# Kernel optimization log

Measured on AMD Instinct MI355X. Metric: run time of the kernel, lower is better.

The kernel has to match this reference:

```python
import jax, jax.numpy as jnp
import numpy as np

B, A, T, C = 8, 16, 512, 256
H = 8
DH = C // H
HID = 4 * C


def setup_inputs() -> dict:
    key = jax.random.key(0)
    ks = jax.random.split(key, 16)
    s = 0.02
    return {
        "x": jax.random.normal(ks[0], (B, A, T, C), jnp.float32),
        "ln1_w": jnp.ones((C,), jnp.float32),
        "ln1_b": jnp.zeros((C,), jnp.float32),
        "qkv_w": jax.random.normal(ks[1], (C, 3 * C), jnp.float32) * s,
        "qkv_b": jnp.zeros((3 * C,), jnp.float32),
        "proj_w": jax.random.normal(ks[2], (C, C), jnp.float32) * s,
        "proj_b": jnp.zeros((C,), jnp.float32),
        "ln2_w": jnp.ones((C,), jnp.float32),
        "ln2_b": jnp.zeros((C,), jnp.float32),
        "fc_w": jax.random.normal(ks[3], (C, HID), jnp.float32) * s,
        "fc_b": jnp.zeros((HID,), jnp.float32),
        "fc2_w": jax.random.normal(ks[4], (HID, C), jnp.float32) * s,
        "fc2_b": jnp.zeros((C,), jnp.float32),
    }


def _layernorm(x, w, b, eps=1e-5):
    mu = jnp.mean(x, axis=-1, keepdims=True)
    var = jnp.var(x, axis=-1, keepdims=True)
    return (x - mu) * jax.lax.rsqrt(var + eps) * w + b


def reference(x, ln1_w, ln1_b, qkv_w, qkv_b, proj_w, proj_b,
              ln2_w, ln2_b, fc_w, fc_b, fc2_w, fc2_b):
    # pre-LN block; note: residuals branch off the *normalized* tensor,
    # exactly as in the source forward().
    xn = _layernorm(x, ln1_w, ln1_b)                       # (B,A,T,C)

    qkv = xn @ qkv_w + qkv_b                               # (B,A,T,3C)
    q, k, v = jnp.split(qkv, 3, axis=-1)
    # (B,A,T,C) -> (B,A,H,T,Dh)
    def heads(t):
        return t.reshape(B, A, T, H, DH).transpose(0, 1, 3, 2, 4)
    q, k, v = heads(q), heads(k), heads(v)

    att = jnp.einsum('bahtd,bahsd->bahts', q, k) / np.sqrt(DH).astype(np.float32)
    att = jax.nn.softmax(att, axis=-1)                     # (B,A,H,T,T)
    y = jnp.einsum('bahts,bahsd->bahtd', att, v)
    y = y.transpose(0, 1, 3, 2, 4).reshape(B, A, T, C)
    y = y @ proj_w + proj_b

    x2 = xn + y
    x2n = _layernorm(x2, ln2_w, ln2_b)
    h = jax.nn.gelu(x2n @ fc_w + fc_b, approximate=False)
    m = h @ fc2_w + fc2_b
    return x2n + m
```

## Files before the change

kernel.cpp:

```cpp
#include <hip/hip_runtime.h>

typedef unsigned short u16;
typedef __attribute__((ext_vector_type(8))) short s16x8;
typedef __attribute__((ext_vector_type(4))) float f32x4;

#define MFMA_BF16(a,b,c) __builtin_amdgcn_mfma_f32_16x16x32_bf16((a),(b),(c),0,0,0)

#define GLL(gp, lp) __builtin_amdgcn_global_load_lds( \
    (const __attribute__((address_space(1))) void*)(gp), \
    (__attribute__((address_space(3))) void*)(lp), 16, 0, 0)

#define PIPE_WAIT_BAR(N) do { \
  asm volatile("s_waitcnt vmcnt(" #N ")" ::: "memory"); \
  __builtin_amdgcn_sched_barrier(0); \
  __builtin_amdgcn_s_barrier(); \
  __builtin_amdgcn_sched_barrier(0); \
} while (0)

#define PIPE_BAR() do { \
  asm volatile("" ::: "memory"); \
  __builtin_amdgcn_sched_barrier(0); \
  __builtin_amdgcn_s_barrier(); \
  __builtin_amdgcn_sched_barrier(0); \
} while (0)

__device__ __forceinline__ float b2f(u16 s){
  union { unsigned u; float f; } v; v.u = ((unsigned)s) << 16; return v.f;
}
__device__ __forceinline__ u16 f2b(float x){
  union { float f; unsigned u; } v; v.f = x;
  unsigned u = v.u;
  return (u16)((u + 0x7FFFu + ((u >> 16) & 1u)) >> 16);
}
__device__ __forceinline__ u16 f2b_trunc(float x){
  union { float f; unsigned u; } v; v.f = x;
  return (u16)(v.u >> 16);
}

__device__ __forceinline__ float gelu_fast(float v){
  float av = fabsf(v) * 0.70710678118654752f;
  float t  = __builtin_amdgcn_rcpf(1.0f + 0.3275911f * av);
  float p  = ((((1.061405429f * t - 1.453152027f) * t + 1.421413741f) * t
               - 0.284496736f) * t + 0.254829592f) * t;
  float erfa = 1.0f - p * __expf(-av * av);
  return 0.5f * v * (1.0f + copysignf(erfa, v));
}

__global__ __launch_bounds__(256) void wconv_all(
    const float* __restrict__ w0, u16* __restrict__ t0,
    const float* __restrict__ w1, u16* __restrict__ t1,
    const float* __restrict__ w2, u16* __restrict__ t2,
    const float* __restrict__ w3, u16* __restrict__ t3)
{
  int bid = blockIdx.x;
  const float* w; u16* t; int K, N, base;
  if (bid < 768)        { w = w0; t = t0; K = 256;  N = 768;  base = bid; }
  else if (bid < 1024)  { w = w1; t = t1; K = 256;  N = 256;  base = bid - 768; }
  else if (bid < 2048)  { w = w2; t = t2; K = 256;  N = 1024; base = bid - 1024; }
  else                  { w = w3; t = t3; K = 1024; N = 256;  base = bid - 2048; }
  int idx = base * 256 + threadIdx.x;
  if (idx >= K * N) return;
  int k = idx / N, n = idx - k * N;
  t[(size_t)n * K + k] = f2b(w[idx]);
}

__global__ __launch_bounds__(256) void ln_f32(const float* __restrict__ in,
    const float* __restrict__ gam, const float* __restrict__ bet, u16* __restrict__ out)
{
  int wv = threadIdx.x >> 6, lane = threadIdx.x & 63;
  size_t row = (size_t)blockIdx.x * 4 + wv;
  float4 u = *(const float4*)(in + row * 256 + lane * 4);
  float s  = u.x + u.y + u.z + u.w;
  float s2 = u.x*u.x + u.y*u.y + u.z*u.z + u.w*u.w;
  #pragma unroll
  for (int off = 32; off; off >>= 1){
    s  += __shfl_xor(s, off);
    s2 += __shfl_xor(s2, off);
  }
  float mean = s * (1.0f/256.0f);
  float var  = s2 * (1.0f/256.0f) - mean*mean;
  float rs   = rsqrtf(var + 1e-5f);
  int c = lane * 4;
  float4 g4 = *(const float4*)(gam + c);
  float4 b4 = *(const float4*)(bet + c);
  ushort4 o;
  o.x = f2b((u.x - mean)*rs*g4.x + b4.x);
  o.y = f2b((u.y - mean)*rs*g4.y + b4.y);
  o.z = f2b((u.z - mean)*rs*g4.z + b4.z);
  o.w = f2b((u.w - mean)*rs*g4.w + b4.w);
  *(ushort4*)(out + row * 256 + c) = o;
}

template<int EPI, int NT>
__global__ __launch_bounds__(256) void gemm128(
    const u16* __restrict__ A, const u16* __restrict__ Bt, const float* __restrict__ bias,
    const u16* __restrict__ res, void* __restrict__ o0v, u16* __restrict__ o1, u16* __restrict__ o2,
    int N, int K)
{
  __shared__ __align__(16) u16 lds[24576];
  int tid = threadIdx.x;
  int w = tid >> 6, lane = tid & 63;
  int quad = lane >> 4, c = lane & 15;
  int bid = blockIdx.x;
  int x = bid & 7, j = bid >> 3;
  int nt = j % NT, mt = (j / NT) * 8 + x;
  int wm = (w >> 1) * 64, wn = (w & 1) * 64;
  const u16* Abase = A + (size_t)mt * 128 * K;
  const u16* Bbase = Bt + (size_t)nt * 128 * K;
  int m0 = tid & 127, jj0 = tid >> 7;
  f32x4 zero = {0.f, 0.f, 0.f, 0.f};
  f32x4 acc[4][4];
  #pragma unroll
  for (int mi = 0; mi < 4; mi++)
    #pragma unroll
    for (int ni = 0; ni < 4; ni++) acc[mi][ni] = zero;

  auto stage = [&](int buf, int k0){
    u16* base = &lds[buf * 8192];
    GLL(Abase + (size_t)m0 * K + k0 + jj0 * 8,       &base[tid * 8]);
    GLL(Abase + (size_t)m0 * K + k0 + (jj0 + 2) * 8, &base[2048 + tid * 8]);
    GLL(Bbase + (size_t)m0 * K + k0 + jj0 * 8,       &base[4096 + tid * 8]);
    GLL(Bbase + (size_t)m0 * K + k0 + (jj0 + 2) * 8, &base[6144 + tid * 8]);
  };
  auto compute = [&](int cb){
    const u16* Lb = &lds[cb * 8192];
    s16x8 af[4], bfr[4];
    #pragma unroll
    for (int mi = 0; mi < 4; mi++)
      af[mi] = *(const s16x8*)&Lb[(quad * 128 + wm + mi * 16 + c) * 8];
    #pragma unroll
    for (int ni = 0; ni < 4; ni++)
      bfr[ni] = *(const s16x8*)&Lb[4096 + (quad * 128 + wn + ni * 16 + c) * 8];
    #pragma unroll
    for (int mi = 0; mi < 4; mi++)
      #pragma unroll
      for (int ni = 0; ni < 4; ni++)
        acc[mi][ni] = MFMA_BF16(af[mi], bfr[ni], acc[mi][ni]);
  };

  stage(0, 0); stage(1, 32); stage(2, 64);
  int cur = 0;
  int k0 = 0;
  for (; k0 + 96 < K; k0 += 32){
    PIPE_WAIT_BAR(8);
    compute(cur);
    PIPE_BAR();
    stage(cur, k0 + 96);
    cur = (cur == 2) ? 0 : cur + 1;
  }
  PIPE_WAIT_BAR(8); compute(cur); cur = (cur == 2) ? 0 : cur + 1;
  PIPE_WAIT_BAR(4); compute(cur); cur = (cur == 2) ? 0 : cur + 1;
  PIPE_WAIT_BAR(0); compute(cur);

  const int LS  = 132;
  const int LSF = 133;
  float* ldsF = (float*)lds;
  int rr = tid >> 3;
  int c7 = tid & 7;

  #pragma unroll
  for (int ch = 0; ch < 4; ch++){
    __syncthreads();
    if ((w >> 1) == (ch >> 1)){
      #pragma unroll
      for (int mi2 = 0; mi2 < 2; mi2++){
        int mi = (ch & 1) * 2 + mi2;
        #pragma unroll
        for (int ni = 0; ni < 4; ni++){
          int col = wn + ni * 16 + c;
          float bv = bias[nt * 128 + col];
          #pragma unroll
          for (int r = 0; r < 4; r++){
            int cr = mi2 * 16 + quad * 4 + r;
            float vv = acc[mi][ni][r] + bv;
            if (EPI == 0){
              int gcol = nt * 128 + col;
              if ((gcol >> 8) == 0) vv *= 0.17677669529663687f;
              lds[cr * LS + col] = f2b(vv);
            } else if (EPI == 2){
              lds[cr * LS + col] = f2b(gelu_fast(vv));
            } else {
              ldsF[cr * LSF + col] = vv;
            }
          }
        }
      }
    }
    __syncthreads();
    int row = mt * 128 + ch * 32 + rr;
    if (EPI == 3){
      #pragma unroll
      for (int jj2 = 0; jj2 < 4; jj2++){
        int colL = c7 * 4 + jj2 * 32;
        size_t gidx = (size_t)row * N + nt * 128 + colL;
        float4 vv = *(const float4*)&ldsF[rr * LSF + colL];
        ushort4 r4 = *(const ushort4*)(res + gidx);
        float4 o4;
        o4.x = vv.x + b2f(r4.x);
        o4.y = vv.y + b2f(r4.y);
        o4.z = vv.z + b2f(r4.z);
        o4.w = vv.w + b2f(r4.w);
        *(float4*)((float*)o0v + gidx) = o4;
      }
    } else {
      #pragma unroll
      for (int jj2 = 0; jj2 < 2; jj2++){
        int colL = c7 * 8 + jj2 * 64;
        uint4 val = *(const uint4*)&lds[rr * LS + colL];
        if (EPI == 0){
          int gcol = nt * 128 + colL;
          int which = gcol >> 8, ccc = gcol & 255;
          int hh = ccc >> 5, d = ccc & 31;
          int ba = row >> 9, t = row & 511;
          size_t idx = (((size_t)(ba * 8 + hh)) * 512 + t) * 32 + d;
          u16* dst = (which == 0) ? (u16*)o0v : ((which == 1) ? o1 : o2);
          *(uint4*)(dst + idx) = val;
        } else {
          *(uint4*)((u16*)o0v + (size_t)row * N + nt * 128 + colL) = val;
        }
      }
    }
  }
}

__global__ __launch_bounds__(256) void proj_ln(
    const u16* __restrict__ A, const u16* __restrict__ Bt, const float* __restrict__ bias,
    const u16* __restrict__ res, const float* __restrict__ gam, const float* __restrict__ bet,
    u16* __restrict__ x2n)
{
  __shared__ __align__(16) u16 lds[20480];
  int tid = threadIdx.x;
  int w = tid >> 6, lane = tid & 63;
  int quad = lane >> 4, c = lane & 15;
  int mt = blockIdx.x;
  int wn = w * 64;
  const u16* Abase = A + (size_t)mt * 64 * 256;
  int an = tid & 63, aj = tid >> 6;
  f32x4 zero = {0.f, 0.f, 0.f, 0.f};
  f32x4 acc[4][4];
  #pragma unroll
  for (int mi = 0; mi < 4; mi++)
    #pragma unroll
    for (int ni = 0; ni < 4; ni++) acc[mi][ni] = zero;

  auto stage = [&](int buf, int k0){
    u16* base = &lds[buf * 10240];
    GLL(Abase + (size_t)an * 256 + k0 + aj * 8, &base[tid * 8]);
    #pragma unroll
    for (int i = 0; i < 4; i++){
      int ci = tid + i * 256;
      int n = ci & 255, jjb = ci >> 8;
      GLL(Bt + (size_t)n * 256 + k0 + jjb * 8, &base[2048 + ci * 8]);
    }
  };
  auto compute = [&](int cb){
    const u16* base = &lds[cb * 10240];
    s16x8 af[4], bfr[4];
    #pragma unroll
    for (int mi = 0; mi < 4; mi++)
      af[mi] = *(const s16x8*)&base[(quad * 64 + mi * 16 + c) * 8];
    #pragma unroll
    for (int ni = 0; ni < 4; ni++)
      bfr[ni] = *(const s16x8*)&base[2048 + (quad * 256 + wn + ni * 16 + c) * 8];
    #pragma unroll
    for (int mi = 0; mi < 4; mi++)
      #pragma unroll
      for (int ni = 0; ni < 4; ni++)
        acc[mi][ni] = MFMA_BF16(af[mi], bfr[ni], acc[mi][ni]);
  };

  stage(0, 0);
  int cur = 0;
  for (int k0 = 32; k0 < 256; k0 += 32){
    stage(cur ^ 1, k0);
    PIPE_WAIT_BAR(5);
    compute(cur);
    PIPE_BAR();
    cur ^= 1;
  }
  PIPE_WAIT_BAR(0);
  compute(cur);
  __syncthreads();

  #pragma unroll
  for (int ni = 0; ni < 4; ni++){
    int col = wn + ni * 16 + c;
    float bv = bias[col];
    #pragma unroll
    for (int mi = 0; mi < 4; mi++){
      #pragma unroll
      for (int r = 0; r < 4; r++){
        int rowL = mi * 16 + quad * 4 + r;
        size_t gidx = ((size_t)mt * 64 + rowL) * 256 + col;
        lds[rowL * 264 + col] = f2b(acc[mi][ni][r] + bv + b2f(res[gidx]));
      }
    }
  }
  __syncthreads();

  int rowL = tid >> 2, part = (tid & 3) * 64;
  float s = 0.f, s2 = 0.f;
  #pragma unroll
  for (int i = 0; i < 16; i++){
    ushort4 u = *(const ushort4*)&lds[rowL * 264 + part + i * 4];
    float v0 = b2f(u.x), v1 = b2f(u.y), v2 = b2f(u.z), v3 = b2f(u.w);
    s  += v0 + v1 + v2 + v3;
    s2 += v0*v0 + v1*v1 + v2*v2 + v3*v3;
  }
  s  += __shfl_xor(s, 1);  s  += __shfl_xor(s, 2);
  s2 += __shfl_xor(s2, 1); s2 += __shfl_xor(s2, 2);
  float mean = s * (1.0f/256.0f);
  float var  = s2 * (1.0f/256.0f) - mean*mean;
  float rs   = rsqrtf(var + 1e-5f);
  size_t orow = ((size_t)mt * 64 + rowL) * 256;
  #pragma unroll
  for (int i = 0; i < 16; i++){
    int col = part + i * 4;
    ushort4 u = *(const ushort4*)&lds[rowL * 264 + col];
    float4 g4 = *(const float4*)(gam + col);
    float4 b4 = *(const float4*)(bet + col);
    ushort4 o;
    o.x = f2b((b2f(u.x) - mean)*rs*g4.x + b4.x);
    o.y = f2b((b2f(u.y) - mean)*rs*g4.y + b4.y);
    o.z = f2b((b2f(u.z) - mean)*rs*g4.z + b4.z);
    o.w = f2b((b2f(u.w) - mean)*rs*g4.w + b4.w);
    *(ushort4*)(x2n + orow + col) = o;
  }
}

__global__ __launch_bounds__(256) void attn_kernel(const u16* __restrict__ q,
    const u16* __restrict__ k, const u16* __restrict__ v, u16* __restrict__ y)
{
  __shared__ __align__(16) u16 ldsK[32 * 36];
  __shared__ __align__(16) u16 ldsV[32 * 36];
  __shared__ __align__(16) u16 ldsp[4][16 * 36];
  int tid = threadIdx.x;
  int w = tid >> 6, lane = tid & 63;
  int quad = lane >> 4, c = lane & 15;
  int bid = blockIdx.x;
  int x = bid & 7, j = bid >> 3;
  int qt = j & 3, bah = (j >> 2) * 8 + x;
  int q0 = qt * 128 + w * 32;
  const u16* qb = q + (size_t)bah * 16384;
  const u16* kb = k + (size_t)bah * 16384;
  const u16* vb = v + (size_t)bah * 16384;
  int krow = tid >> 3, kcol = (tid & 7) * 4;
  int vd = tid & 31,  vs = (tid >> 5) * 4;

  s16x8 qf0 = *(const s16x8*)(qb + (q0 + c) * 32 + quad * 8);
  s16x8 qf1 = *(const s16x8*)(qb + (q0 + 16 + c) * 32 + quad * 8);
  float l0[4] = {0.f,0.f,0.f,0.f}, l1[4] = {0.f,0.f,0.f,0.f};
  f32x4 o00 = {0,0,0,0}, o01 = {0,0,0,0}, o10 = {0,0,0,0}, o11 = {0,0,0,0};
  f32x4 zero = {0,0,0,0};

  for (int s0 = 0; s0 < 512; s0 += 32){
    uint2 kr = *(const uint2*)(kb + (s0 + krow) * 32 + kcol);
    short4 vr;
    vr.x = (short)vb[(s0 + vs)     * 32 + vd];
    vr.y = (short)vb[(s0 + vs + 1) * 32 + vd];
    vr.z = (short)vb[(s0 + vs + 2) * 32 + vd];
    vr.w = (short)vb[(s0 + vs + 3) * 32 + vd];
    __syncthreads();
    *(uint2*)&ldsK[krow * 36 + kcol] = kr;
    *(short4*)&ldsV[vd * 36 + vs]   = vr;
    __syncthreads();

    s16x8 kf0 = *(const s16x8*)&ldsK[c * 36 + quad * 8];
    s16x8 kf1 = *(const s16x8*)&ldsK[(16 + c) * 36 + quad * 8];
    s16x8 vf0 = *(const s16x8*)&ldsV[c * 36 + quad * 8];
    s16x8 vf1 = *(const s16x8*)&ldsV[(16 + c) * 36 + quad * 8];

    f32x4 S0 = MFMA_BF16(qf0, kf0, zero);
    f32x4 S1 = MFMA_BF16(qf0, kf1, zero);
    #pragma unroll
    for (int r = 0; r < 4; r++){
      float p0 = __expf(S0[r]), p1 = __expf(S1[r]);
      l0[r] += p0 + p1;
      int prow = quad * 4 + r;
      ldsp[w][prow * 36 + c]      = f2b_trunc(p0);
      ldsp[w][prow * 36 + 16 + c] = f2b_trunc(p1);
    }
    s16x8 pf = *(const s16x8*)&ldsp[w][c * 36 + quad * 8];
    o00 = MFMA_BF16(pf, vf0, o00);
    o01 = MFMA_BF16(pf, vf1, o01);

    S0 = MFMA_BF16(qf1, kf0, zero);
    S1 = MFMA_BF16(qf1, kf1, zero);
    #pragma unroll
    for (int r = 0; r < 4; r++){
      float p0 = __expf(S0[r]), p1 = __expf(S1[r]);
      l1[r] += p0 + p1;
      int prow = quad * 4 + r;
      ldsp[w][prow * 36 + c]      = f2b_trunc(p0);
      ldsp[w][prow * 36 + 16 + c] = f2b_trunc(p1);
    }
    pf = *(const s16x8*)&ldsp[w][c * 36 + quad * 8];
    o10 = MFMA_BF16(pf, vf0, o10);
    o11 = MFMA_BF16(pf, vf1, o11);
  }

  #pragma unroll
  for (int r = 0; r < 4; r++){
    #pragma unroll
    for (int off = 8; off; off >>= 1){
      l0[r] += __shfl_xor(l0[r], off);
      l1[r] += __shfl_xor(l1[r], off);
    }
  }

  int ba = bah >> 3, hh = bah & 7;
  #pragma unroll
  for (int r = 0; r < 4; r++){
    int t0 = q0 + quad * 4 + r;
    float inv0 = 1.0f / l0[r], inv1 = 1.0f / l1[r];
    size_t base0 = ((size_t)(ba * 512 + t0)) * 256 + hh * 32;
    size_t base1 = base0 + 16 * 256;
    y[base0 + c]      = f2b(o00[r] * inv0);
    y[base0 + 16 + c] = f2b(o01[r] * inv0);
    y[base1 + c]      = f2b(o10[r] * inv1);
    y[base1 + 16 + c] = f2b(o11[r] * inv1);
  }
}

extern "C" void kernel_launch(void* const* d_in, const int* in_sizes, int n_in,
                              void* d_out, int out_size, void* d_ws, size_t ws_size,
                              hipStream_t stream)
{
  const float* x      = (const float*)d_in[0];
  const float* ln1_w  = (const float*)d_in[1];
  const float* ln1_b  = (const float*)d_in[2];
  const float* qkv_w  = (const float*)d_in[3];
  const float* qkv_b  = (const float*)d_in[4];
  const float* proj_w = (const float*)d_in[5];
  const float* proj_b = (const float*)d_in[6];
  const float* ln2_w  = (const float*)d_in[7];
  const float* ln2_b  = (const float*)d_in[8];
  const float* fc_w   = (const float*)d_in[9];
  const float* fc_b   = (const float*)d_in[10];
  const float* fc2_w  = (const float*)d_in[11];
  const float* fc2_b  = (const float*)d_in[12];
  float* out = (float*)d_out;
  char* ws = (char*)d_ws;

  u16* xn   = (u16*)ws;
  u16* qb   = (u16*)(ws + (size_t)33554432);
  u16* kb   = qb + 16777216;
  u16* vb   = kb + 16777216;
  u16* yb   = vb + 16777216;
  u16* hb   = qb;
  u16* x2n  = (u16*)(ws + (size_t)173015040);
  u16* wqkvT  = (u16*)(ws + (size_t)206569472);
  u16* wprojT = wqkvT + 196608;
  u16* wfcT   = wprojT + 65536;
  u16* wfc2T  = wfcT + 262144;

  wconv_all<<<3072, 256, 0, stream>>>(qkv_w, wqkvT, proj_w, wprojT, fc_w, wfcT, fc2_w, wfc2T);

  ln_f32<<<16384, 256, 0, stream>>>(x, ln1_w, ln1_b, xn);
  gemm128<0,6><<<3072, 256, 0, stream>>>(xn, wqkvT, qkv_b, nullptr, qb, kb, vb, 768, 256);
  attn_kernel<<<4096, 256, 0, stream>>>(qb, kb, vb, yb);
  proj_ln<<<1024, 256, 0, stream>>>(yb, wprojT, proj_b, xn, ln2_w, ln2_b, x2n);
  gemm128<2,8><<<4096, 256, 0, stream>>>(x2n, wfcT, fc_b, nullptr, hb, nullptr, nullptr, 1024, 256);
  gemm128<3,2><<<1024, 256, 0, stream>>>(hb, wfc2T, fc2_b, x2n, out, nullptr, nullptr, 256, 1024);
}
```

Measured before the change: 526.7 us.

## Fuse FFN fc+GELU+fc2 into one kernel keeping hidden activations in LDS

Replaces the two FFN GEMM launches with a single kernel. Each block of 64 rows computes 128-wide hidden chunks with GELU, keeps them in swizzled LDS, and accumulates the fc2 output in registers. It then adds the bias and the x2n residual before storing fp32. This removes the global write and read of the 64 MB hidden tensor and one launch. In exchange, weight tiles are read directly from global memory without LDS staging or pipelining, only 1024 blocks run, and there is more register pressure.

```diff
diff --git a/kernel.cpp b/kernel.cpp
--- a/kernel.cpp
+++ b/kernel.cpp
@@ -153,8 +153,6 @@
   PIPE_WAIT_BAR(0); compute(cur);
 
   const int LS  = 132;
-  const int LSF = 133;
-  float* ldsF = (float*)lds;
   int rr = tid >> 3;
   int c7 = tid & 7;
 
@@ -177,10 +175,6 @@
               int gcol = nt * 128 + col;
               if ((gcol >> 8) == 0) vv *= 0.17677669529663687f;
               lds[cr * LS + col] = f2b(vv);
-            } else if (EPI == 2){
-              lds[cr * LS + col] = f2b(gelu_fast(vv));
-            } else {
-              ldsF[cr * LSF + col] = vv;
             }
           }
         }
@@ -188,38 +182,157 @@
     }
     __syncthreads();
     int row = mt * 128 + ch * 32 + rr;
-    if (EPI == 3){
-      #pragma unroll
-      for (int jj2 = 0; jj2 < 4; jj2++){
-        int colL = c7 * 4 + jj2 * 32;
-        size_t gidx = (size_t)row * N + nt * 128 + colL;
-        float4 vv = *(const float4*)&ldsF[rr * LSF + colL];
-        ushort4 r4 = *(const ushort4*)(res + gidx);
-        float4 o4;
-        o4.x = vv.x + b2f(r4.x);
-        o4.y = vv.y + b2f(r4.y);
-        o4.z = vv.z + b2f(r4.z);
-        o4.w = vv.w + b2f(r4.w);
-        *(float4*)((float*)o0v + gidx) = o4;
-      }
-    } else {
-      #pragma unroll
-      for (int jj2 = 0; jj2 < 2; jj2++){
-        int colL = c7 * 8 + jj2 * 64;
-        uint4 val = *(const uint4*)&lds[rr * LS + colL];
-        if (EPI == 0){
-          int gcol = nt * 128 + colL;
-          int which = gcol >> 8, ccc = gcol & 255;
-          int hh = ccc >> 5, d = ccc & 31;
-          int ba = row >> 9, t = row & 511;
-          size_t idx = (((size_t)(ba * 8 + hh)) * 512 + t) * 32 + d;
-          u16* dst = (which == 0) ? (u16*)o0v : ((which == 1) ? o1 : o2);
-          *(uint4*)(dst + idx) = val;
-        } else {
-          *(uint4*)((u16*)o0v + (size_t)row * N + nt * 128 + colL) = val;
+    #pragma unroll
+    for (int jj2 = 0; jj2 < 2; jj2++){
+      int colL = c7 * 8 + jj2 * 64;
+      uint4 val = *(const uint4*)&lds[rr * LS + colL];
+      if (EPI == 0){
+        int gcol = nt * 128 + colL;
+        int which = gcol >> 8, ccc = gcol & 255;
+        int hh = ccc >> 5, d = ccc & 31;
+        int ba = row >> 9, t = row & 511;
+        size_t idx = (((size_t)(ba * 8 + hh)) * 512 + t) * 32 + d;
+        u16* dst = (which == 0) ? (u16*)o0v : ((which == 1) ? o1 : o2);
+        *(uint4*)(dst + idx) = val;
+      } else {
+        *(uint4*)((u16*)o0v + (size_t)row * N + nt * 128 + colL) = val;
+      }
+    }
+  }
+}
+
+__global__ __launch_bounds__(256) void ffn_fused(
+    const u16* __restrict__ x2n, const u16* __restrict__ fcT, const float* __restrict__ fcb,
+    const u16* __restrict__ fc2T, const float* __restrict__ fc2b, float* __restrict__ out)
+{
+  __shared__ __align__(16) u16 lds[24576];
+  int tid = threadIdx.x;
+  int w = tid >> 6, lane = tid & 63;
+  int quad = lane >> 4, c = lane & 15;
+  int mt = blockIdx.x;
+  const u16* Abase = x2n + (size_t)mt * 64 * 256;
+  char* ldsc = (char*)lds;
+  char* hl   = (char*)lds + 32768;
+
+  #pragma unroll
+  for (int i = 0; i < 8; i++){
+    int ci = i * 256 + tid;
+    int row = ci >> 5, slot = ci & 31;
+    int glow = (slot * 16) ^ ((row & 7) << 4);
+    GLL((const char*)Abase + row * 512 + glow, ldsc + ci * 16);
+  }
+  f32x4 zero = {0.f, 0.f, 0.f, 0.f};
+  f32x4 acc2[4][4];
+  #pragma unroll
+  for (int mi = 0; mi < 4; mi++)
+    #pragma unroll
+    for (int ni = 0; ni < 4; ni++) acc2[mi][ni] = zero;
+  PIPE_WAIT_BAR(0);
+
+  for (int hc = 0; hc < 8; hc++){
+    f32x4 acc1[4][2];
+    #pragma unroll
+    for (int mi = 0; mi < 4; mi++){ acc1[mi][0] = zero; acc1[mi][1] = zero; }
+    #pragma unroll
+    for (int ks = 0; ks < 8; ks++){
+      s16x8 af[4], bf1[2];
+      #pragma unroll
+      for (int ni = 0; ni < 2; ni++){
+        int n = hc * 128 + w * 32 + ni * 16 + c;
+        bf1[ni] = *(const s16x8*)(fcT + (size_t)n * 256 + ks * 32 + quad * 8);
+      }
+      #pragma unroll
+      for (int mi = 0; mi < 4; mi++){
+        int row = mi * 16 + c;
+        int kb = (ks * 64 + quad * 16) ^ ((row & 7) << 4);
+        af[mi] = *(const s16x8*)(ldsc + row * 512 + kb);
+      }
+      #pragma unroll
+      for (int mi = 0; mi < 4; mi++){
+        acc1[mi][0] = MFMA_BF16(af[mi], bf1[0], acc1[mi][0]);
+        acc1[mi][1] = MFMA_BF16(af[mi], bf1[1], acc1[mi][1]);
+      }
+    }
+    __syncthreads();
+    #pragma unroll
+    for (int ni = 0; ni < 2; ni++){
+      int colc = w * 32 + ni * 16 + c;
+      float bv = fcb[hc * 128 + colc];
+      #pragma unroll
+      for (int mi = 0; mi < 4; mi++){
+        #pragma unroll
+        for (int r = 0; r < 4; r++){
+          int row = mi * 16 + quad * 4 + r;
+          int by = (colc * 2) ^ ((row & 15) << 4);
+          *(u16*)(hl + row * 256 + by) = f2b(gelu_fast(acc1[mi][ni][r] + bv));
         }
       }
     }
+    __syncthreads();
+    #pragma unroll
+    for (int ks = 0; ks < 4; ks++){
+      s16x8 ha[4], bf2[4];
+      #pragma unroll
+      for (int ni = 0; ni < 4; ni++){
+        int n = w * 64 + ni * 16 + c;
+        bf2[ni] = *(const s16x8*)(fc2T + (size_t)n * 1024 + hc * 128 + ks * 32 + quad * 8);
+      }
+      #pragma unroll
+      for (int mi = 0; mi < 4; mi++){
+        int row = mi * 16 + c;
+        int kb = (ks * 64 + quad * 16) ^ ((row & 15) << 4);
+        ha[mi] = *(const s16x8*)(hl + row * 256 + kb);
+      }
+      #pragma unroll
+      for (int mi = 0; mi < 4; mi++)
+        #pragma unroll
+        for (int ni = 0; ni < 4; ni++)
+          acc2[mi][ni] = MFMA_BF16(ha[mi], bf2[ni], acc2[mi][ni]);
+    }
+  }
+
+  #pragma unroll
+  for (int ni = 0; ni < 4; ni++){
+    int col = w * 64 + ni * 16 + c;
+    float bv = fc2b[col];
+    #pragma unroll
+    for (int mi = 0; mi < 4; mi++){
+      #pragma unroll
+      for (int r = 0; r < 4; r++){
+        int row = mi * 16 + quad * 4 + r;
+        int by = (col * 2) ^ ((row & 7) << 4);
+        u16 xv = *(const u16*)(ldsc + row * 512 + by);
+        acc2[mi][ni][r] += bv + b2f(xv);
+      }
+    }
+  }
+  __syncthreads();
+
+  float* ldsF = (float*)lds;
+  const int LSO = 260;
+  int rr = tid >> 3, c8 = tid & 7;
+  #pragma unroll
+  for (int ch = 0; ch < 2; ch++){
+    #pragma unroll
+    for (int mi2 = 0; mi2 < 2; mi2++){
+      int mi = ch * 2 + mi2;
+      #pragma unroll
+      for (int ni = 0; ni < 4; ni++){
+        #pragma unroll
+        for (int r = 0; r < 4; r++){
+          int crow = mi2 * 16 + quad * 4 + r;
+          ldsF[crow * LSO + w * 64 + ni * 16 + c] = acc2[mi][ni][r];
+        }
+      }
+    }
+    __syncthreads();
+    size_t rb = ((size_t)mt * 64 + ch * 32 + rr) * 256;
+    #pragma unroll
+    for (int jj = 0; jj < 8; jj++){
+      int col = c8 * 4 + jj * 32;
+      *(float4*)(out + rb + col) = *(const float4*)&ldsF[rr * LSO + col];
+    }
+    __syncthreads();
   }
 }
 
@@ -447,7 +560,6 @@
   u16* kb   = qb + 16777216;
   u16* vb   = kb + 16777216;
   u16* yb   = vb + 16777216;
-  u16* hb   = qb;
   u16* x2n  = (u16*)(ws + (size_t)173015040);
   u16* wqkvT  = (u16*)(ws + (size_t)206569472);
   u16* wprojT = wqkvT + 196608;
@@ -460,6 +572,5 @@
   gemm128<0,6><<<3072, 256, 0, stream>>>(xn, wqkvT, qkv_b, nullptr, qb, kb, vb, 768, 256);
   attn_kernel<<<4096, 256, 0, stream>>>(qb, kb, vb, yb);
   proj_ln<<<1024, 256, 0, stream>>>(yb, wprojT, proj_b, xn, ln2_w, ln2_b, x2n);
-  gemm128<2,8><<<4096, 256, 0, stream>>>(x2n, wfcT, fc_b, nullptr, hb, nullptr, nullptr, 1024, 256);
-  gemm128<3,2><<<1024, 256, 0, stream>>>(hb, wfc2T, fc2_b, x2n, out, nullptr, nullptr, 256, 1024);
-}
+  ffn_fused<<<1024, 256, 0, stream>>>(x2n, wfcT, fc_b, wfc2T, fc2_b, out);
+}
```

Measured after the change: 537.3 us. +2.0%, slower.

## Fuse FFN fc and fc2 GEMMs into one kernel keeping hidden activations in LDS

Applied to the files above, without the earlier changes.

Replaces the two separate FFN GEMM launches with one fused kernel. Each block takes 64 rows of x2n, computes the GELU hidden activations in 128-wide chunks into double-buffered LDS, and accumulates the fc2 output directly, adding bias and the residual at the end. It uses 32x32x16 MFMA and reads weights straight from global memory without LDS staging. This removes the global write and re-read of the large hidden tensor and one launch. In exchange, weight reads are uncached per block, occupancy is limited by 64 KB of LDS, and the unused EPI 2/3 epilogue paths are dropped from gemm128.

```diff
diff --git a/kernel.cpp b/kernel.cpp
--- a/kernel.cpp
+++ b/kernel.cpp
@@ -3,8 +3,10 @@
 typedef unsigned short u16;
 typedef __attribute__((ext_vector_type(8))) short s16x8;
 typedef __attribute__((ext_vector_type(4))) float f32x4;
-
-#define MFMA_BF16(a,b,c) __builtin_amdgcn_mfma_f32_16x16x32_bf16((a),(b),(c),0,0,0)
+typedef __attribute__((ext_vector_type(16))) float f32x16;
+
+#define MFMA_BF16(a,b,c)   __builtin_amdgcn_mfma_f32_16x16x32_bf16((a),(b),(c),0,0,0)
+#define MFMA32_BF16(a,b,c) __builtin_amdgcn_mfma_f32_32x32x16_bf16((a),(b),(c),0,0,0)
 
 #define GLL(gp, lp) __builtin_amdgcn_global_load_lds( \
     (const __attribute__((address_space(1))) void*)(gp), \
@@ -153,8 +155,6 @@
   PIPE_WAIT_BAR(0); compute(cur);
 
   const int LS  = 132;
-  const int LSF = 133;
-  float* ldsF = (float*)lds;
   int rr = tid >> 3;
   int c7 = tid & 7;
 
@@ -177,10 +177,6 @@
               int gcol = nt * 128 + col;
               if ((gcol >> 8) == 0) vv *= 0.17677669529663687f;
               lds[cr * LS + col] = f2b(vv);
-            } else if (EPI == 2){
-              lds[cr * LS + col] = f2b(gelu_fast(vv));
-            } else {
-              ldsF[cr * LSF + col] = vv;
             }
           }
         }
@@ -188,37 +184,112 @@
     }
     __syncthreads();
     int row = mt * 128 + ch * 32 + rr;
-    if (EPI == 3){
-      #pragma unroll
-      for (int jj2 = 0; jj2 < 4; jj2++){
-        int colL = c7 * 4 + jj2 * 32;
-        size_t gidx = (size_t)row * N + nt * 128 + colL;
-        float4 vv = *(const float4*)&ldsF[rr * LSF + colL];
-        ushort4 r4 = *(const ushort4*)(res + gidx);
-        float4 o4;
-        o4.x = vv.x + b2f(r4.x);
-        o4.y = vv.y + b2f(r4.y);
-        o4.z = vv.z + b2f(r4.z);
-        o4.w = vv.w + b2f(r4.w);
-        *(float4*)((float*)o0v + gidx) = o4;
+    #pragma unroll
+    for (int jj2 = 0; jj2 < 2; jj2++){
+      int colL = c7 * 8 + jj2 * 64;
+      uint4 val = *(const uint4*)&lds[rr * LS + colL];
+      if (EPI == 0){
+        int gcol = nt * 128 + colL;
+        int which = gcol >> 8, ccc = gcol & 255;
+        int hh = ccc >> 5, d = ccc & 31;
+        int ba = row >> 9, t = row & 511;
+        size_t idx = (((size_t)(ba * 8 + hh)) * 512 + t) * 32 + d;
+        u16* dst = (which == 0) ? (u16*)o0v : ((which == 1) ? o1 : o2);
+        *(uint4*)(dst + idx) = val;
+      } else {
+        *(uint4*)((u16*)o0v + (size_t)row * N + nt * 128 + colL) = val;
       }
-    } else {
-      #pragma unroll
-      for (int jj2 = 0; jj2 < 2; jj2++){
-        int colL = c7 * 8 + jj2 * 64;
-        uint4 val = *(const uint4*)&lds[rr * LS + colL];
-        if (EPI == 0){
-          int gcol = nt * 128 + colL;
-          int which = gcol >> 8, ccc = gcol & 255;
-          int hh = ccc >> 5, d = ccc & 31;
-          int ba = row >> 9, t = row & 511;
-          size_t idx = (((size_t)(ba * 8 + hh)) * 512 + t) * 32 + d;
-          u16* dst = (which == 0) ? (u16*)o0v : ((which == 1) ? o1 : o2);
-          *(uint4*)(dst + idx) = val;
-        } else {
-          *(uint4*)((u16*)o0v + (size_t)row * N + nt * 128 + colL) = val;
-        }
-      }
+    }
+  }
+}
+
+__global__ __launch_bounds__(512, 4) void ffn_fused(
+    const u16* __restrict__ x2n, const u16* __restrict__ fcT, const float* __restrict__ fcb,
+    const u16* __restrict__ fc2T, const float* __restrict__ fc2b, float* __restrict__ out)
+{
+  __shared__ __align__(16) u16 lds[32768];
+  int tid = threadIdx.x;
+  int w = tid >> 6, lane = tid & 63;
+  int l31 = lane & 31, hi = lane >> 5;
+  int lsw = (l31 & 15) << 4;
+  int mt = blockIdx.x;
+  const u16* Abase = x2n + (size_t)mt * 64 * 256;
+  char* ldsc = (char*)lds;
+  char* h0   = (char*)lds + 32768;
+  char* h1   = (char*)lds + 49152;
+  int mt1 = w >> 2, nt1 = w & 3;
+
+  #pragma unroll
+  for (int i = 0; i < 4; i++){
+    int ci = i * 512 + tid;
+    int row = ci >> 5, slot = ci & 31;
+    int glow = (slot * 16) ^ ((row & 15) << 4);
+    GLL((const char*)Abase + row * 512 + glow, ldsc + ci * 16);
+  }
+  f32x16 accA, accB;
+  #pragma unroll
+  for (int i = 0; i < 16; i++){ accA[i] = 0.f; accB[i] = 0.f; }
+
+  auto gemm1 = [&](int hcx, char* hw){
+    f32x16 acc1;
+    #pragma unroll
+    for (int i = 0; i < 16; i++) acc1[i] = 0.f;
+    const u16* fA = fcT + (size_t)(hcx * 128 + nt1 * 32 + l31) * 256 + hi * 8;
+    const char* xB = ldsc + (mt1 * 32 + l31) * 512;
+    #pragma unroll
+    for (int ks = 0; ks < 16; ks++){
+      s16x8 af = *(const s16x8*)(fA + ks * 16);
+      s16x8 bf = *(const s16x8*)(xB + ((ks * 32 + hi * 16) ^ lsw));
+      acc1 = MFMA32_BF16(af, bf, acc1);
+    }
+    int m  = mt1 * 32 + l31;
+    int nb0 = nt1 * 32 + hi * 4;
+    #pragma unroll
+    for (int rq = 0; rq < 4; rq++){
+      int nn = nb0 + rq * 8;
+      float4 bb = *(const float4*)(fcb + hcx * 128 + nn);
+      short4 pk;
+      pk.x = (short)f2b(gelu_fast(acc1[rq*4+0] + bb.x));
+      pk.y = (short)f2b(gelu_fast(acc1[rq*4+1] + bb.y));
+      pk.z = (short)f2b(gelu_fast(acc1[rq*4+2] + bb.z));
+      pk.w = (short)f2b(gelu_fast(acc1[rq*4+3] + bb.w));
+      *(short4*)(hw + m * 256 + ((nn * 2) ^ lsw)) = pk;
+    }
+  };
+  auto gemm2 = [&](int hcx, const char* hr){
+    const u16* fB = fc2T + (size_t)(w * 32 + l31) * 1024 + hcx * 128 + hi * 8;
+    #pragma unroll
+    for (int ks = 0; ks < 8; ks++){
+      s16x8 bf2 = *(const s16x8*)(fB + ks * 16);
+      int ko = (ks * 32 + hi * 16) ^ lsw;
+      s16x8 ha0 = *(const s16x8*)(hr + l31 * 256 + ko);
+      s16x8 ha1 = *(const s16x8*)(hr + (32 + l31) * 256 + ko);
+      accA = MFMA32_BF16(ha0, bf2, accA);
+      accB = MFMA32_BF16(ha1, bf2, accB);
+    }
+  };
+
+  PIPE_WAIT_BAR(0);
+  gemm1(0, h0);
+  __syncthreads();
+  for (int hc = 0; hc < 8; hc++){
+    const char* hr = (hc & 1) ? h1 : h0;
+    char* hw       = (hc & 1) ? h0 : h1;
+    if (hc < 7) gemm1(hc + 1, hw);
+    gemm2(hc, hr);
+    __syncthreads();
+  }
+
+  int n = w * 32 + l31;
+  float bv = fc2b[n];
+  #pragma unroll
+  for (int mt2 = 0; mt2 < 2; mt2++){
+    #pragma unroll
+    for (int r = 0; r < 16; r++){
+      int row = mt2 * 32 + (r & 3) + 8 * (r >> 2) + 4 * hi;
+      u16 xv = *(const u16*)(ldsc + row * 512 + ((n * 2) ^ ((row & 15) << 4)));
+      float vv = (mt2 ? accB[r] : accA[r]) + bv + b2f(xv);
+      out[((size_t)mt * 64 + row) * 256 + n] = vv;
     }
   }
 }
@@ -447,7 +518,6 @@
   u16* kb   = qb + 16777216;
   u16* vb   = kb + 16777216;
   u16* yb   = vb + 16777216;
-  u16* hb   = qb;
   u16* x2n  = (u16*)(ws + (size_t)173015040);
   u16* wqkvT  = (u16*)(ws + (size_t)206569472);
   u16* wprojT = wqkvT + 196608;
@@ -460,6 +530,5 @@
   gemm128<0,6><<<3072, 256, 0, stream>>>(xn, wqkvT, qkv_b, nullptr, qb, kb, vb, 768, 256);
   attn_kernel<<<4096, 256, 0, stream>>>(qb, kb, vb, yb);
   proj_ln<<<1024, 256, 0, stream>>>(yb, wprojT, proj_b, xn, ln2_w, ln2_b, x2n);
-  gemm128<2,8><<<4096, 256, 0, stream>>>(x2n, wfcT, fc_b, nullptr, hb, nullptr, nullptr, 1024, 256);
-  gemm128<3,2><<<1024, 256, 0, stream>>>(hb, wfc2T, fc2_b, x2n, out, nullptr, nullptr, 256, 1024);
-}
+  ffn_fused<<<1024, 512, 0, stream>>>(x2n, wfcT, fc_b, wfc2T, fc2_b, out);
+}
```

After: 532.4 us. No clear change (+1.1%).
